# Kernel tuning notes

Hardware: AMD Instinct MI355X
Metric: run time of the kernel (lower is better)

The kernel has to match this reference:

```python
import jax, jax.numpy as jnp
import numpy as np

N = 50000       # nodes
E = 800000      # edges
IN = 256        # input channels
H = 4           # heads
C = 64          # hidden channels per head
NEG_SLOPE = 0.2 # PyG GATConv default LeakyReLU slope
EPS = 1e-16


def setup_inputs() -> dict:
    key = jax.random.key(0)
    k_x, k_e, k_w, k_as, k_ad = jax.random.split(key, 5)
    x = jax.random.normal(k_x, (N, IN), dtype=jnp.float32)
    edge_index = jax.random.randint(k_e, (2, E), 0, N, dtype=jnp.int64)
    # GATConv params: glorot-style scale
    W = jax.random.normal(k_w, (IN, H * C), dtype=jnp.float32) * (1.0 / np.sqrt(IN))
    att_src = jax.random.normal(k_as, (H, C), dtype=jnp.float32) * (1.0 / np.sqrt(C))
    att_dst = jax.random.normal(k_ad, (H, C), dtype=jnp.float32) * (1.0 / np.sqrt(C))
    return {"x": x, "edge_index": edge_index, "W": W, "att_src": att_src, "att_dst": att_dst}


def reference(x, edge_index, W, att_src, att_dst):
    src, dst = edge_index[0], edge_index[1]
    # linear projection, split heads: [N, H, C]
    xh = (x @ W).reshape(N, H, C)
    # per-node attention halves: [N, H]
    a_src = jnp.einsum('nhc,hc->nh', xh, att_src)
    a_dst = jnp.einsum('nhc,hc->nh', xh, att_dst)
    # per-edge logits with LeakyReLU: [E, H]
    alpha = a_src[src] + a_dst[dst]
    alpha = jnp.where(alpha >= 0, alpha, NEG_SLOPE * alpha)
    # segment softmax over destination nodes
    m = jax.ops.segment_max(alpha, dst, num_segments=N)          # [N, H]
    ex = jnp.exp(alpha - m[dst])                                  # [E, H]
    denom = jax.ops.segment_sum(ex, dst, num_segments=N)         # [N, H]
    att = ex / (denom[dst] + EPS)                                 # [E, H]
    # weighted message scatter-add: [N, H, C] -> concat heads [N, H*C]
    msg = att[:, :, None] * xh[src]                               # [E, H, C]
    out = jax.ops.segment_sum(msg, dst, num_segments=N)
    out = out.reshape(N, H * C)
    return (out, att)
```

## Files before the change

### kernel.cpp

```cpp
#include <hip/hip_runtime.h>
#include <math.h>

#define IN_CH   256
#define HC      256
#define H_HEADS 4
#define NEG_SLOPE 0.2f
#define LOG2E   1.44269504088896f
#define DEFER_THR 12.0f

typedef __attribute__((ext_vector_type(8))) short short8;
typedef __attribute__((ext_vector_type(4))) short short4v;
typedef __attribute__((ext_vector_type(4))) float float4v;

__device__ __forceinline__ float bf2f(unsigned short b) {
    return __uint_as_float(((unsigned)b) << 16);
}
__device__ __forceinline__ unsigned short f2bf(float f) {
    unsigned u = __float_as_uint(f);
    u += 0x7fffu + ((u >> 16) & 1u);
    return (unsigned short)(u >> 16);
}
__device__ __forceinline__ float lrelu(float a) {
    return a >= 0.f ? a : NEG_SLOPE * a;
}
__device__ __forceinline__ float fexp2(float a) {
    return __builtin_amdgcn_exp2f(a);
}


__global__ void prep_w(const float* __restrict__ w,
                       unsigned short* __restrict__ wt) {
    int idx = blockIdx.x * 256 + threadIdx.x;
    int k = idx >> 8, c = idx & 255;
    wt[(size_t)c * 256 + k] = f2bf(w[idx]);
}

__global__ __launch_bounds__(256) void gemm_xh(const float* __restrict__ x,
                                               const unsigned short* __restrict__ wt,
                                               const float* __restrict__ att_s,
                                               const float* __restrict__ att_d,
                                               unsigned short* __restrict__ xh_bf,
                                               float* __restrict__ a_src,
                                               float* __restrict__ a_dst, int N) {
    __shared__ __attribute__((aligned(16))) unsigned char lds_a[16384];
    int tid  = threadIdx.x;
    int wave = tid >> 6;
    int lane = tid & 63;
    int quad = lane >> 4;
    int l16  = lane & 15;
    int rb   = blockIdx.x * 16;

#pragma unroll
    for (int pass = 0; pass < 2; ++pass) {
        int s  = pass * 256 + tid;
        int kc = s >> 4;
        int m  = s & 15;
        int grow = rb + m; if (grow >= N) grow = N - 1;
        const float* gp = x + (size_t)grow * IN_CH + kc * 8;
        float4v f0 = *(const float4v*)gp;
        float4v f1 = *(const float4v*)(gp + 4);
        short8 hi, lo;
#pragma unroll
        for (int j = 0; j < 4; ++j) {
            unsigned short h0 = f2bf(f0[j]);
            hi[j] = (short)h0;
            lo[j] = (short)f2bf(f0[j] - bf2f(h0));
            unsigned short h1 = f2bf(f1[j]);
            hi[4 + j] = (short)h1;
            lo[4 + j] = (short)f2bf(f1[j] - bf2f(h1));
        }
        *(short8*)(lds_a + (size_t)s * 16) = hi;
        *(short8*)(lds_a + 8192 + (size_t)s * 16) = lo;
    }
    __syncthreads();

    float4v acc[4] = {};
    const unsigned short* wt_base = wt + ((size_t)wave * 64 + l16) * IN_CH;
#pragma unroll
    for (int k0 = 0; k0 < 8; ++k0) {
        int kc   = k0 * 4 + quad;
        int slot = kc * 16 + l16;
        short8 a_hi = *(const short8*)(lds_a + slot * 16);
        short8 a_lo = *(const short8*)(lds_a + 8192 + slot * 16);
#pragma unroll
        for (int ct = 0; ct < 4; ++ct) {
            short8 bh = *(const short8*)(wt_base + (size_t)ct * 16 * IN_CH
                                         + k0 * 32 + quad * 8);
            acc[ct] = __builtin_amdgcn_mfma_f32_16x16x32_bf16(a_lo, bh, acc[ct], 0, 0, 0);
            acc[ct] = __builtin_amdgcn_mfma_f32_16x16x32_bf16(a_hi, bh, acc[ct], 0, 0, 0);
        }
    }

    int cb = wave;
    float ps[4] = {0.f, 0.f, 0.f, 0.f};
    float pd[4] = {0.f, 0.f, 0.f, 0.f};
#pragma unroll
    for (int ct = 0; ct < 4; ++ct) {
        float as_c = att_s[cb * 64 + ct * 16 + l16] * LOG2E;
        float ad_c = att_d[cb * 64 + ct * 16 + l16] * LOG2E;
#pragma unroll
        for (int r = 0; r < 4; ++r) {
            float v = acc[ct][r];
            int grow = rb + quad * 4 + r;
            if (grow < N)
                xh_bf[(size_t)grow * HC + cb * 64 + ct * 16 + l16] = f2bf(v);
            ps[r] += v * as_c;
            pd[r] += v * ad_c;
        }
    }
#pragma unroll
    for (int off = 1; off < 16; off <<= 1) {
#pragma unroll
        for (int r = 0; r < 4; ++r) {
            ps[r] += __shfl_xor(ps[r], off);
            pd[r] += __shfl_xor(pd[r], off);
        }
    }
    if (l16 == 0) {
#pragma unroll
        for (int r = 0; r < 4; ++r) {
            int grow = rb + quad * 4 + r;
            if (grow < N) {
                a_src[(size_t)grow * 4 + cb] = ps[r];
                a_dst[(size_t)grow * 4 + cb] = pd[r];
            }
        }
    }
}

__global__ __launch_bounds__(256) void deg_count(const int* __restrict__ ei,
                                                 int* __restrict__ deg, int E) {
    int e = blockIdx.x * 256 + threadIdx.x;
    if (e >= E) return;
    atomicAdd(deg + ei[E + e], 1);
}


__global__ __launch_bounds__(256) void scan_part(const int* __restrict__ deg,
                                                 int* __restrict__ part, int N) {
    int t = threadIdx.x;
    int base = blockIdx.x * 1024 + t * 4;
    int s = 0;
    if (base + 4 <= N) {
        int4 v = *(const int4*)(deg + base);
        s = v.x + v.y + v.z + v.w;
    } else {
#pragma unroll
        for (int j = 0; j < 4; ++j)
            if (base + j < N) s += deg[base + j];
    }
#pragma unroll
    for (int off = 1; off < 64; off <<= 1) s += __shfl_xor(s, off);
    __shared__ int ws[4];
    if ((t & 63) == 0) ws[t >> 6] = s;
    __syncthreads();
    if (t == 0) part[blockIdx.x] = ws[0] + ws[1] + ws[2] + ws[3];
}

__global__ __launch_bounds__(256) void scan_final(const int* __restrict__ deg,
                                                  const int* __restrict__ part,
                                                  int* __restrict__ rowptr,
                                                  int* __restrict__ cursor, int N) {
    __shared__ int sm[256];
    __shared__ int wsum[4];
    int t = threadIdx.x;
    int bacc = 0;
    for (int j = t; j < blockIdx.x; j += 256) bacc += part[j];
#pragma unroll
    for (int off = 1; off < 64; off <<= 1) bacc += __shfl_xor(bacc, off);
    if ((t & 63) == 0) wsum[t >> 6] = bacc;

    int base = blockIdx.x * 1024 + t * 4;
    int v0 = 0, v1 = 0, v2 = 0, v3 = 0;
    if (base + 4 <= N) {
        int4 v = *(const int4*)(deg + base);
        v0 = v.x; v1 = v.y; v2 = v.z; v3 = v.w;
    } else {
        if (base + 0 < N) v0 = deg[base + 0];
        if (base + 1 < N) v1 = deg[base + 1];
        if (base + 2 < N) v2 = deg[base + 2];
        if (base + 3 < N) v3 = deg[base + 3];
    }
    int s = v0 + v1 + v2 + v3;
    sm[t] = s;
    __syncthreads();
    for (int off = 1; off < 256; off <<= 1) {
        int tmp = (t >= off) ? sm[t - off] : 0;
        __syncthreads();
        sm[t] += tmp;
        __syncthreads();
    }
    int boff = wsum[0] + wsum[1] + wsum[2] + wsum[3];
    int run = boff + sm[t] - s;
    int r0 = run, r1 = r0 + v0, r2 = r1 + v1, r3 = r2 + v2;
    if (base + 4 <= N) {
        *(int4*)(rowptr + base) = (int4){r0, r1, r2, r3};
        *(int4*)(cursor + base) = (int4){r0, r1, r2, r3};
    } else {
        if (base + 0 < N) { rowptr[base + 0] = r0; cursor[base + 0] = r0; }
        if (base + 1 < N) { rowptr[base + 1] = r1; cursor[base + 1] = r1; }
        if (base + 2 < N) { rowptr[base + 2] = r2; cursor[base + 2] = r2; }
        if (base + 3 < N) { rowptr[base + 3] = r3; cursor[base + 3] = r3; }
    }
}

__global__ __launch_bounds__(256) void fill_csr(const int* __restrict__ ei,
                                                const float* __restrict__ a_src,
                                                const float* __restrict__ a_dst,
                                                int* __restrict__ cursor,
                                                int* __restrict__ csr_src,
                                                float* __restrict__ csr_al,
                                                float* __restrict__ al_e, int E) {
    int e = blockIdx.x * 256 + threadIdx.x;
    if (e >= E) return;
    int s = ei[e], d = ei[E + e];
    float4v as = *(const float4v*)(a_src + (size_t)s * 4);
    float4v ad = *(const float4v*)(a_dst + (size_t)d * 4);
    float4v al;
#pragma unroll
    for (int h = 0; h < 4; ++h) al[h] = lrelu(as[h] + ad[h]);
    int slot = atomicAdd(cursor + d, 1);
    csr_src[slot] = s;
    *(float4v*)(csr_al + (size_t)slot * 4) = al;
    *(float4v*)(al_e + (size_t)e * 4) = al;
}

__global__ __launch_bounds__(256) void gat_gather(const int* __restrict__ csr_src,
                                                  const float* __restrict__ csr_al,
                                                  const int* __restrict__ rowptr,
                                                  const int* __restrict__ deg,
                                                  const unsigned short* __restrict__ xh_bf,
                                                  float* __restrict__ out,
                                                  float* __restrict__ pack, int N) {
    int wave = threadIdx.x >> 6, lane = threadIdx.x & 63;
    int d = blockIdx.x * 4 + wave;
    if (d >= N) return;
    int h = lane >> 4;
    int start = rowptr[d], cnt = deg[d];

    if (cnt == 0) {
        *(float4v*)(out + (size_t)d * HC + lane * 4) = (float4v){0.f, 0.f, 0.f, 0.f};
        if ((lane & 15) == 0) {
            pack[(size_t)d * 8 + h]     = 0.f;
            pack[(size_t)d * 8 + 4 + h] = 0.f;
        }
        return;
    }

    float mE = -INFINITY, lE = 0.f, mO = -INFINITY, lO = 0.f;
    float4v accE = {0.f, 0.f, 0.f, 0.f}, accO = {0.f, 0.f, 0.f, 0.f};

    int s2 = 0, s3 = 0;
    float alE = 0.f, alO = 0.f;
    short4v xvE = {}, xvO = {};
    {
        int s0 = csr_src[start];
        alE = csr_al[(size_t)start * 4 + h];
        xvE = *(const short4v*)(xh_bf + (size_t)s0 * HC + lane * 4);
    }
    if (cnt > 1) {
        int s1 = csr_src[start + 1];
        alO = csr_al[(size_t)(start + 1) * 4 + h];
        xvO = *(const short4v*)(xh_bf + (size_t)s1 * HC + lane * 4);
    }
    if (cnt > 2) s2 = csr_src[start + 2];
    if (cnt > 3) s3 = csr_src[start + 3];

    for (int i = 0; i < cnt; i += 2) {
        float alE_n = 0.f, alO_n = 0.f;
        short4v xvE_n = {}, xvO_n = {};
        if (i + 2 < cnt) {
            alE_n = csr_al[(size_t)(start + i + 2) * 4 + h];
            xvE_n = *(const short4v*)(xh_bf + (size_t)s2 * HC + lane * 4);
        }
        if (i + 3 < cnt) {
            alO_n = csr_al[(size_t)(start + i + 3) * 4 + h];
            xvO_n = *(const short4v*)(xh_bf + (size_t)s3 * HC + lane * 4);
        }
        int s4 = (i + 4 < cnt) ? csr_src[start + i + 4] : 0;
        int s5 = (i + 5 < cnt) ? csr_src[start + i + 5] : 0;

        bool haveO = (i + 1 < cnt);
        bool ok = (alE <= mE + DEFER_THR);
        if (haveO) ok = ok && (alO <= mO + DEFER_THR);
        if (__all(ok)) {
            float p = fexp2(alE - mE);
            lE += p;
#pragma unroll
            for (int j = 0; j < 4; ++j)
                accE[j] += p * bf2f((unsigned short)xvE[j]);
            if (haveO) {
                float q = fexp2(alO - mO);
                lO += q;
#pragma unroll
                for (int j = 0; j < 4; ++j)
                    accO[j] += q * bf2f((unsigned short)xvO[j]);
            }
        } else {
            {
                float mn = fmaxf(mE, alE);
                float sc = fexp2(mE - mn);
                float p  = fexp2(alE - mn);
                lE = lE * sc + p;
#pragma unroll
                for (int j = 0; j < 4; ++j)
                    accE[j] = accE[j] * sc + p * bf2f((unsigned short)xvE[j]);
                mE = mn;
            }
            if (haveO) {
                float mn = fmaxf(mO, alO);
                float sc = fexp2(mO - mn);
                float p  = fexp2(alO - mn);
                lO = lO * sc + p;
#pragma unroll
                for (int j = 0; j < 4; ++j)
                    accO[j] = accO[j] * sc + p * bf2f((unsigned short)xvO[j]);
                mO = mn;
            }
        }
        alE = alE_n; xvE = xvE_n; alO = alO_n; xvO = xvO_n;
        s2 = s4; s3 = s5;
    }
    float mm = fmaxf(mE, mO);
    float sE = fexp2(mE - mm), sO = fexp2(mO - mm);
    float l  = lE * sE + lO * sO;
    float inv = 1.f / (l + 1e-16f);
    float4v o;
#pragma unroll
    for (int j = 0; j < 4; ++j) o[j] = (accE[j] * sE + accO[j] * sO) * inv;
    *(float4v*)(out + (size_t)d * HC + lane * 4) = o;
    if ((lane & 15) == 0) {
        pack[(size_t)d * 8 + h]     = mm;
        pack[(size_t)d * 8 + 4 + h] = inv;
    }
}

__global__ __launch_bounds__(256) void att_edge(const int* __restrict__ ei,
                                                const float* __restrict__ al_e,
                                                const float* __restrict__ pack,
                                                float* __restrict__ att_out, int E) {
    int e = blockIdx.x * 256 + threadIdx.x;
    if (e >= E) return;
    int d = ei[E + e];
    float4v al = *(const float4v*)(al_e + (size_t)e * 4);
    float4v mm = *(const float4v*)(pack + (size_t)d * 8);
    float4v gg = *(const float4v*)(pack + (size_t)d * 8 + 4);
    float4v o;
#pragma unroll
    for (int h = 0; h < 4; ++h)
        o[h] = fexp2(al[h] - mm[h]) * gg[h];
    *(float4v*)(att_out + (size_t)e * 4) = o;
}

extern "C" void kernel_launch(void* const* d_in, const int* in_sizes, int n_in,
                              void* d_out, int out_size, void* d_ws, size_t ws_size,
                              hipStream_t stream) {
    const float* x     = (const float*)d_in[0];
    const int*   ei    = (const int*)d_in[1];
    const float* W     = (const float*)d_in[2];
    const float* att_s = (const float*)d_in[3];
    const float* att_d = (const float*)d_in[4];

    const int N = in_sizes[0] / IN_CH;
    const int E = in_sizes[1] / 2;

    char* ws = (char*)d_ws;
    size_t off = 0;
    unsigned short* xh_bf = (unsigned short*)(ws + off); off += (size_t)N * HC * 2;
    unsigned short* wt    = (unsigned short*)(ws + off); off += (size_t)IN_CH * HC * 2;
    float* a_src = (float*)(ws + off); off += (size_t)N * H_HEADS * 4;
    float* a_dst = (float*)(ws + off); off += (size_t)N * H_HEADS * 4;
    float* pack  = (float*)(ws + off); off += (size_t)N * 8 * 4;
    int* rowptr  = (int*)(ws + off); off += (size_t)N * 4;
    int* cursor  = (int*)(ws + off); off += (size_t)N * 4;
    int* csr_src = (int*)(ws + off); off += (size_t)E * 4;
    float* csr_al = (float*)(ws + off); off += (size_t)E * 4 * 4;
    float* al_e   = (float*)(ws + off); off += (size_t)E * 4 * 4;
    int* part    = (int*)(ws + off); off += 1024 * 4;
    size_t zoff = off;
    int* deg     = (int*)(ws + off); off += (size_t)N * 4;

    float* out     = (float*)d_out;
    float* out_att = out + (size_t)N * HC;

    (void)hipMemsetAsync(ws + zoff, 0, off - zoff, stream);

    const int NB = (N + 1023) / 1024;

    prep_w<<<256, 256, 0, stream>>>(W, wt);
    deg_count<<<(E + 255) / 256, 256, 0, stream>>>(ei, deg, E);
    gemm_xh<<<(N + 15) / 16, 256, 0, stream>>>(x, wt, att_s, att_d,
                                               xh_bf, a_src, a_dst, N);
    scan_part<<<NB, 256, 0, stream>>>(deg, part, N);
    scan_final<<<NB, 256, 0, stream>>>(deg, part, rowptr, cursor, N);
    fill_csr<<<(E + 255) / 256, 256, 0, stream>>>(ei, a_src, a_dst, cursor,
                                                  csr_src, csr_al, al_e, E);
    gat_gather<<<(N + 3) / 4, 256, 0, stream>>>(csr_src, csr_al, rowptr, deg,
                                                xh_bf, out, pack, N);
    att_edge<<<(E + 255) / 256, 256, 0, stream>>>(ei, al_e, pack, out_att, E);
}
```

Baseline: 324.2 us.

## Process two destination nodes per wave with 16-byte gathers and precomputed byte offsets

The gather kernel now gives each half-wave (32 lanes) its own destination node. Each lane loads 8 bf16 values (16 bytes) per neighbor row instead of 4, and the edge-loop branches are made uniform by padding to the larger degree of the two nodes, using -inf logits for padded slots. The CSR now stores source row byte offsets (s<<9), so no multiply is needed per edge. This aims for wider memory transactions and half the waves, at the cost of idle iterations when the two paired nodes have different degrees and more registers per lane.

```diff
diff --git a/kernel.cpp b/kernel.cpp
--- a/kernel.cpp
+++ b/kernel.cpp
@@ -7,6 +7,7 @@
 #define NEG_SLOPE 0.2f
 #define LOG2E   1.44269504088896f
 #define DEFER_THR 12.0f
+#define MINIT   -3.0e38f
 
 typedef __attribute__((ext_vector_type(8))) short short8;
 typedef __attribute__((ext_vector_type(4))) short short4v;
@@ -208,7 +209,7 @@
                                                 const float* __restrict__ a_src,
                                                 const float* __restrict__ a_dst,
                                                 int* __restrict__ cursor,
-                                                int* __restrict__ csr_src,
+                                                int* __restrict__ csr_off,
                                                 float* __restrict__ csr_al,
                                                 float* __restrict__ al_e, int E) {
     int e = blockIdx.x * 256 + threadIdx.x;
@@ -220,12 +221,12 @@
 #pragma unroll
     for (int h = 0; h < 4; ++h) al[h] = lrelu(as[h] + ad[h]);
     int slot = atomicAdd(cursor + d, 1);
-    csr_src[slot] = s;
+    csr_off[slot] = s << 9;
     *(float4v*)(csr_al + (size_t)slot * 4) = al;
     *(float4v*)(al_e + (size_t)e * 4) = al;
 }
 
-__global__ __launch_bounds__(256) void gat_gather(const int* __restrict__ csr_src,
+__global__ __launch_bounds__(256) void gat_gather(const int* __restrict__ csr_off,
                                                   const float* __restrict__ csr_al,
                                                   const int* __restrict__ rowptr,
                                                   const int* __restrict__ deg,
@@ -233,105 +234,88 @@
                                                   float* __restrict__ out,
                                                   float* __restrict__ pack, int N) {
     int wave = threadIdx.x >> 6, lane = threadIdx.x & 63;
-    int d = blockIdx.x * 4 + wave;
-    if (d >= N) return;
-    int h = lane >> 4;
-    int start = rowptr[d], cnt = deg[d];
-
-    if (cnt == 0) {
-        *(float4v*)(out + (size_t)d * HC + lane * 4) = (float4v){0.f, 0.f, 0.f, 0.f};
-        if ((lane & 15) == 0) {
-            pack[(size_t)d * 8 + h]     = 0.f;
-            pack[(size_t)d * 8 + 4 + h] = 0.f;
-        }
-        return;
-    }
-
-    float mE = -INFINITY, lE = 0.f, mO = -INFINITY, lO = 0.f;
-    float4v accE = {0.f, 0.f, 0.f, 0.f}, accO = {0.f, 0.f, 0.f, 0.f};
-
-    int s2 = 0, s3 = 0;
-    float alE = 0.f, alO = 0.f;
-    short4v xvE = {}, xvO = {};
-    {
-        int s0 = csr_src[start];
-        alE = csr_al[(size_t)start * 4 + h];
-        xvE = *(const short4v*)(xh_bf + (size_t)s0 * HC + lane * 4);
-    }
-    if (cnt > 1) {
-        int s1 = csr_src[start + 1];
-        alO = csr_al[(size_t)(start + 1) * 4 + h];
-        xvO = *(const short4v*)(xh_bf + (size_t)s1 * HC + lane * 4);
-    }
-    if (cnt > 2) s2 = csr_src[start + 2];
-    if (cnt > 3) s3 = csr_src[start + 3];
-
-    for (int i = 0; i < cnt; i += 2) {
-        float alE_n = 0.f, alO_n = 0.f;
-        short4v xvE_n = {}, xvO_n = {};
-        if (i + 2 < cnt) {
-            alE_n = csr_al[(size_t)(start + i + 2) * 4 + h];
-            xvE_n = *(const short4v*)(xh_bf + (size_t)s2 * HC + lane * 4);
-        }
-        if (i + 3 < cnt) {
-            alO_n = csr_al[(size_t)(start + i + 3) * 4 + h];
-            xvO_n = *(const short4v*)(xh_bf + (size_t)s3 * HC + lane * 4);
-        }
-        int s4 = (i + 4 < cnt) ? csr_src[start + i + 4] : 0;
-        int s5 = (i + 5 < cnt) ? csr_src[start + i + 5] : 0;
-
-        bool haveO = (i + 1 < cnt);
-        bool ok = (alE <= mE + DEFER_THR);
-        if (haveO) ok = ok && (alO <= mO + DEFER_THR);
+    int half = lane >> 5;
+    int l32  = lane & 31;
+    int h    = l32 >> 3;
+    int d    = blockIdx.x * 8 + wave * 2 + half;
+    bool dv  = d < N;
+    int dc   = dv ? d : N - 1;
+    int start = rowptr[dc];
+    int cnt   = dv ? deg[dc] : 0;
+    int cntMax = max(cnt, __shfl_xor(cnt, 32));
+
+    const char* xb = (const char*)xh_bf;
+    int lboff = l32 * 16;
+
+    float mE = MINIT, lE = 0.f, mO = MINIT, lO = 0.f;
+    float accE[8] = {0.f, 0.f, 0.f, 0.f, 0.f, 0.f, 0.f, 0.f};
+    float accO[8] = {0.f, 0.f, 0.f, 0.f, 0.f, 0.f, 0.f, 0.f};
+
+#define LOFF(idx) (((idx) < cnt) ? csr_off[start + (idx)] : 0)
+#define LAL(idx)  (((idx) < cnt) ? csr_al[(size_t)(start + (idx)) * 4 + h] : -INFINITY)
+
+    int oE = LOFF(0), oO = LOFF(1);
+    float alE = LAL(0), alO = LAL(1);
+    short8 xvE = *(const short8*)(xb + (size_t)oE + lboff);
+    short8 xvO = *(const short8*)(xb + (size_t)oO + lboff);
+    int oE2 = LOFF(2), oO2 = LOFF(3);
+
+    for (int i = 0; i < cntMax; i += 2) {
+        float alE_n = LAL(i + 2), alO_n = LAL(i + 3);
+        short8 xvE_n = *(const short8*)(xb + (size_t)oE2 + lboff);
+        short8 xvO_n = *(const short8*)(xb + (size_t)oO2 + lboff);
+        int oE3 = LOFF(i + 4), oO3 = LOFF(i + 5);
+
+        bool ok = (alE <= mE + DEFER_THR) && (alO <= mO + DEFER_THR);
         if (__all(ok)) {
             float p = fexp2(alE - mE);
-            lE += p;
-#pragma unroll
-            for (int j = 0; j < 4; ++j)
+            float q = fexp2(alO - mO);
+            lE += p; lO += q;
+#pragma unroll
+            for (int j = 0; j < 8; ++j) {
                 accE[j] += p * bf2f((unsigned short)xvE[j]);
-            if (haveO) {
-                float q = fexp2(alO - mO);
-                lO += q;
-#pragma unroll
-                for (int j = 0; j < 4; ++j)
-                    accO[j] += q * bf2f((unsigned short)xvO[j]);
+                accO[j] += q * bf2f((unsigned short)xvO[j]);
             }
         } else {
-            {
-                float mn = fmaxf(mE, alE);
-                float sc = fexp2(mE - mn);
-                float p  = fexp2(alE - mn);
-                lE = lE * sc + p;
-#pragma unroll
-                for (int j = 0; j < 4; ++j)
-                    accE[j] = accE[j] * sc + p * bf2f((unsigned short)xvE[j]);
-                mE = mn;
+            float mnE = fmaxf(mE, alE);
+            float scE = fexp2(mE - mnE);
+            float pE  = fexp2(alE - mnE);
+            lE = lE * scE + pE;
+            float mnO = fmaxf(mO, alO);
+            float scO = fexp2(mO - mnO);
+            float pO  = fexp2(alO - mnO);
+            lO = lO * scO + pO;
+#pragma unroll
+            for (int j = 0; j < 8; ++j) {
+                accE[j] = accE[j] * scE + pE * bf2f((unsigned short)xvE[j]);
+                accO[j] = accO[j] * scO + pO * bf2f((unsigned short)xvO[j]);
             }
-            if (haveO) {
-                float mn = fmaxf(mO, alO);
-                float sc = fexp2(mO - mn);
-                float p  = fexp2(alO - mn);
-                lO = lO * sc + p;
-#pragma unroll
-                for (int j = 0; j < 4; ++j)
-                    accO[j] = accO[j] * sc + p * bf2f((unsigned short)xvO[j]);
-                mO = mn;
-            }
-        }
-        alE = alE_n; xvE = xvE_n; alO = alO_n; xvO = xvO_n;
-        s2 = s4; s3 = s5;
-    }
+            mE = mnE; mO = mnO;
+        }
+        alE = alE_n; alO = alO_n; xvE = xvE_n; xvO = xvO_n;
+        oE2 = oE3; oO2 = oO3;
+    }
+#undef LOFF
+#undef LAL
+
     float mm = fmaxf(mE, mO);
     float sE = fexp2(mE - mm), sO = fexp2(mO - mm);
     float l  = lE * sE + lO * sO;
     float inv = 1.f / (l + 1e-16f);
-    float4v o;
-#pragma unroll
-    for (int j = 0; j < 4; ++j) o[j] = (accE[j] * sE + accO[j] * sO) * inv;
-    *(float4v*)(out + (size_t)d * HC + lane * 4) = o;
-    if ((lane & 15) == 0) {
-        pack[(size_t)d * 8 + h]     = mm;
-        pack[(size_t)d * 8 + 4 + h] = inv;
+    if (dv) {
+        float4v o0, o1;
+#pragma unroll
+        for (int j = 0; j < 4; ++j) {
+            o0[j] = (accE[j] * sE + accO[j] * sO) * inv;
+            o1[j] = (accE[4 + j] * sE + accO[4 + j] * sO) * inv;
+        }
+        float* orow = out + (size_t)d * HC + l32 * 8;
+        *(float4v*)orow = o0;
+        *(float4v*)(orow + 4) = o1;
+        if ((l32 & 7) == 0) {
+            pack[(size_t)d * 8 + h]     = mm;
+            pack[(size_t)d * 8 + 4 + h] = inv;
+        }
     }
 }
 
@@ -373,7 +357,7 @@
     float* pack  = (float*)(ws + off); off += (size_t)N * 8 * 4;
     int* rowptr  = (int*)(ws + off); off += (size_t)N * 4;
     int* cursor  = (int*)(ws + off); off += (size_t)N * 4;
-    int* csr_src = (int*)(ws + off); off += (size_t)E * 4;
+    int* csr_off = (int*)(ws + off); off += (size_t)E * 4;
     float* csr_al = (float*)(ws + off); off += (size_t)E * 4 * 4;
     float* al_e   = (float*)(ws + off); off += (size_t)E * 4 * 4;
     int* part    = (int*)(ws + off); off += 1024 * 4;
@@ -394,8 +378,8 @@
     scan_part<<<NB, 256, 0, stream>>>(deg, part, N);
     scan_final<<<NB, 256, 0, stream>>>(deg, part, rowptr, cursor, N);
     fill_csr<<<(E + 255) / 256, 256, 0, stream>>>(ei, a_src, a_dst, cursor,
-                                                  csr_src, csr_al, al_e, E);
-    gat_gather<<<(N + 3) / 4, 256, 0, stream>>>(csr_src, csr_al, rowptr, deg,
+                                                  csr_off, csr_al, al_e, E);
+    gat_gather<<<(N + 7) / 8, 256, 0, stream>>>(csr_off, csr_al, rowptr, deg,
                                                 xh_bf, out, pack, N);
     att_edge<<<(E + 255) / 256, 256, 0, stream>>>(ei, al_e, pack, out_att, E);
 }
```

Result: no change. 322.6 us (-0.5%).
